# Kernel tuning notes

Hardware: AMD Instinct MI355X
Metric: run time of the kernel (lower is better)

Reference implementation:

```python
import jax, jax.numpy as jnp
import numpy as np

B, T, C, H = 4, 4096, 1024, 16

def setup_inputs() -> dict:
    key = jax.random.key(0)
    k1, k2, k3, k4 = jax.random.split(key, 4)
    return {
        "x": jax.random.normal(k1, (B, T, C), dtype=jnp.float32),
        "W_attn": jax.random.normal(k2, (C, C), dtype=jnp.float32) * 0.02,
        "b_attn": jnp.zeros((C,), dtype=jnp.float32),
        "W_proj": jax.random.normal(k3, (C, C), dtype=jnp.float32) * 0.02,
        "b_proj": jnp.zeros((C,), dtype=jnp.float32),
        "temp": jnp.ones((H, 1), dtype=jnp.float32),
        "n_head": H,
    }

def reference(x, W_attn, b_attn, W_proj, b_proj, temp, n_head):
    Bb, Tt, Cc = x.shape
    D = Cc // n_head
    # c_attn (torch Linear: x @ W.T + b)
    w = x @ W_attn.T + b_attn                         # (B,T,C)
    w = w.reshape(Bb, Tt, n_head, D).transpose(0, 2, 1, 3)  # (B,H,T,D)
    # F.normalize over token axis (dim=-2), eps=1e-12
    norm = jnp.maximum(jnp.sqrt(jnp.sum(w * w, axis=-2, keepdims=True)), 1e-12)
    w_normed = w / norm
    tmp = jnp.sum(w_normed ** 2, axis=-1) * temp      # (B,H,T) * (H,1) -> (B,H,T)
    Pi = jax.nn.softmax(tmp, axis=1)                  # softmax over heads
    Pi_prob = Pi / (jnp.sum(Pi, axis=-1, keepdims=True) + 1e-8)  # (B,H,T)
    dots = jnp.einsum('bht,bhtd->bhd', Pi_prob, w ** 2)          # (B,H,D)
    attn = 1.0 / (1.0 + dots)                         # (B,H,D)
    y = -(w * Pi[..., None]) * attn[:, :, None, :]    # (B,H,T,D)
    y = y.transpose(0, 2, 1, 3).reshape(Bb, Tt, Cc)
    return y @ W_proj.T + b_proj
```

## Files before the change

### kernel.cpp

```cpp
#include <hip/hip_runtime.h>
#include <hip/hip_bf16.h>

#define BB 4
#define TT 4096
#define CC 1024
#define HH 16
#define DD 64

typedef __attribute__((ext_vector_type(8))) short short8;
typedef __attribute__((ext_vector_type(8))) __bf16 bf16x8;
typedef __attribute__((ext_vector_type(4))) float f32x4;

static __device__ __forceinline__ unsigned short f2bf(float f) {
    unsigned int u = __builtin_bit_cast(unsigned int, f);
    unsigned int r = (u + 0x7FFFu + ((u >> 16) & 1u)) >> 16;
    return (unsigned short)r;
}
static __device__ __forceinline__ float bf2f(unsigned short h) {
    return __builtin_bit_cast(float, ((unsigned int)h) << 16);
}
static __device__ __forceinline__ bf16x8 cvt8(f32x4 a, f32x4 b) {
    bf16x8 r;
    r[0] = (__bf16)a[0]; r[1] = (__bf16)a[1]; r[2] = (__bf16)a[2]; r[3] = (__bf16)a[3];
    r[4] = (__bf16)b[0]; r[5] = (__bf16)b[1]; r[6] = (__bf16)b[2]; r[7] = (__bf16)b[3];
    return r;
}

__global__ void k_f32_to_bf16(const float* __restrict__ src,
                              unsigned short* __restrict__ dst, int n4) {
    int i = blockIdx.x * 256 + threadIdx.x;
    if (i >= n4) return;
    float4 v = ((const float4*)src)[i];
    ushort4 o;
    o.x = f2bf(v.x); o.y = f2bf(v.y); o.z = f2bf(v.z); o.w = f2bf(v.w);
    ((ushort4*)dst)[i] = o;
}

#define GBM 128
#define GBN 128
#define GBK 32

static __device__ __forceinline__ void stage_b16t(
    const unsigned short* __restrict__ Gbase, unsigned short* lbase,
    int k0, int K, int tid)
{
    #pragma unroll
    for (int q = 0; q < 2; ++q) {
        int c = q * 256 + tid;
        int r = c >> 2;
        int j = c & 3;
        int srcj = (j - (r >> 1)) & 3;
        const unsigned short* g = Gbase + (size_t)r * K + k0 + srcj * 8;
        __builtin_amdgcn_global_load_lds(
            (const __attribute__((address_space(1))) void*)g,
            (__attribute__((address_space(3))) void*)(lbase + c * 8), 16, 0, 0);
    }
}

static __device__ __forceinline__ void stage_a32t(
    const float* __restrict__ Gbase, unsigned short* lbase,
    int k0, int K, int tid)
{
    #pragma unroll
    for (int q = 0; q < 4; ++q) {
        int c = q * 256 + tid;
        int r = c >> 3;
        int j = c & 7;
        int srcj = (j - r) & 7;
        const float* g = Gbase + (size_t)r * K + k0 + srcj * 4;
        __builtin_amdgcn_global_load_lds(
            (const __attribute__((address_space(1))) void*)g,
            (__attribute__((address_space(3))) void*)(lbase + c * 8), 16, 0, 0);
    }
}

template<int MODE>
__global__ __launch_bounds__(256, 2)
void k_gemm128(const void* __restrict__ Asrc,
               const unsigned short* __restrict__ B,
               const float* __restrict__ bias,
               void* __restrict__ Cout,
               float* __restrict__ S,
               int M, int N, int K)
{
    constexpr int AREG = (MODE == 0) ? 8192 : 4096;
    __shared__ unsigned short lds[AREG + 4096];
    const int tid  = threadIdx.x;
    const int wave = tid >> 6;
    const int lane = tid & 63;
    const int wr = wave >> 1;
    const int wc = wave & 1;
    const int fr = lane & 15;
    const int hi = lane >> 4;

    const int wg  = blockIdx.x;
    const int swz = (wg & 7) * 128 + (wg >> 3);
    const int bn  = swz & 7;
    const int bm  = swz >> 3;
    const int b   = bm >> 5;

    const float* Af32 = (const float*)Asrc + (size_t)(bm * GBM) * K;
    const unsigned short* Ab16 = (const unsigned short*)Asrc + (size_t)(bm * GBM) * K;
    const unsigned short* Bbase = B +
        ((size_t)((MODE == 1 ? b * N : 0) + bn * GBN)) * K;

    const int nt = K / GBK;

    const int slB  = (hi + (fr >> 1)) & 3;
    const int aoff = (wr * 64 + fr) * 32 + slB * 8;
    const int boff = AREG + (wc * 64 + fr) * 32 + slB * 8;
    const int sl0  = (2 * hi + fr) & 7;
    const int sl1  = (2 * hi + 1 + fr) & 7;
    const int arowf = (wr * 64 + fr) * 32;

    f32x4 acc[4][4] = {};

    for (int kt = 0; kt < nt; ++kt) {
        const int k0 = kt * GBK;
        if (MODE == 0) stage_a32t(Af32, lds, k0, K, tid);
        else           stage_b16t(Ab16, lds, k0, K, tid);
        stage_b16t(Bbase, lds + AREG, k0, K, tid);
        __syncthreads();

        bf16x8 af[4]; short8 bfr[4];
        #pragma unroll
        for (int i = 0; i < 4; ++i) bfr[i] = *(const short8*)&lds[boff + i * 512];
        if (MODE == 0) {
            const float* fbuf = (const float*)lds;
            #pragma unroll
            for (int mi = 0; mi < 4; ++mi)
                af[mi] = cvt8(*(const f32x4*)&fbuf[arowf + mi * 512 + sl0 * 4],
                              *(const f32x4*)&fbuf[arowf + mi * 512 + sl1 * 4]);
        } else {
            #pragma unroll
            for (int mi = 0; mi < 4; ++mi)
                af[mi] = __builtin_bit_cast(bf16x8, *(const short8*)&lds[aoff + mi * 512]);
        }

        #pragma unroll
        for (int mi = 0; mi < 4; ++mi)
            #pragma unroll
            for (int ni = 0; ni < 4; ++ni)
                acc[mi][ni] = __builtin_amdgcn_mfma_f32_16x16x32_bf16(
                    af[mi], __builtin_bit_cast(bf16x8, bfr[ni]),
                    acc[mi][ni], 0, 0, 0);
        __syncthreads();
    }

    const int cg = fr;
    const int rg = hi * 4;
    float* sblk = (float*)&lds[0];
    if (MODE == 0) {
        if (tid < GBN) sblk[tid] = 0.f;
        __syncthreads();
    }
    float csum[4] = {};
    #pragma unroll
    for (int mi = 0; mi < 4; ++mi) {
        #pragma unroll
        for (int ni = 0; ni < 4; ++ni) {
            int col = bn * GBN + wc * 64 + ni * 16 + cg;
            float bv = bias[col];
            #pragma unroll
            for (int j = 0; j < 4; ++j) {
                int row = bm * GBM + wr * 64 + mi * 16 + rg + j;
                float v = acc[mi][ni][j] + bv;
                if (MODE == 0) {
                    ((unsigned short*)Cout)[(size_t)row * N + col] = f2bf(v);
                    csum[ni] += v * v;
                } else {
                    ((float*)Cout)[(size_t)row * N + col] = v;
                }
            }
        }
    }
    if (MODE == 0) {
        #pragma unroll
        for (int ni = 0; ni < 4; ++ni)
            atomicAdd(&sblk[wc * 64 + ni * 16 + cg], csum[ni]);
        __syncthreads();
        if (tid < GBN) atomicAdd(&S[b * CC + bn * GBN + tid], sblk[tid]);
    }
}

__global__ __launch_bounds__(256)
void k_row_softmax(unsigned short* __restrict__ w16, const float* __restrict__ S,
                   const float* __restrict__ temp,
                   float* __restrict__ dotsU, float* __restrict__ sumPi)
{
    __shared__ float dots_local[CC];
    __shared__ float sPi_local[HH];
    const int tid  = threadIdx.x;
    const int wave = tid >> 6;
    const int lane = tid & 63;
    const int bb   = blockIdx.x >> 7;
    const int tile = blockIdx.x & 127;

    for (int c = tid; c < CC; c += 256) dots_local[c] = 0.f;
    if (tid < HH) sPi_local[tid] = 0.f;
    __syncthreads();

    const int g3 = lane >> 3;
    const int li = lane & 7;

    float inv[2][8], tsc[2];
    #pragma unroll
    for (int q = 0; q < 2; ++q) {
        int c = q * 512 + lane * 8;
        const float4* sp = (const float4*)&S[bb * CC + c];
        float4 s0 = sp[0], s1 = sp[1];
        inv[q][0] = 1.f / fmaxf(s0.x, 1e-24f); inv[q][1] = 1.f / fmaxf(s0.y, 1e-24f);
        inv[q][2] = 1.f / fmaxf(s0.z, 1e-24f); inv[q][3] = 1.f / fmaxf(s0.w, 1e-24f);
        inv[q][4] = 1.f / fmaxf(s1.x, 1e-24f); inv[q][5] = 1.f / fmaxf(s1.y, 1e-24f);
        inv[q][6] = 1.f / fmaxf(s1.z, 1e-24f); inv[q][7] = 1.f / fmaxf(s1.w, 1e-24f);
        tsc[q] = temp[q * 8 + g3];
    }

    float dacc[2][8] = {};
    float sPiAcc[2] = {};

    for (int i = 0; i < 8; ++i) {
        int t = tile * 32 + wave * 8 + i;
        unsigned short* row = w16 + ((size_t)bb * TT + t) * CC;
        float wf[2][8];
        float pq[2];
        #pragma unroll
        for (int q = 0; q < 2; ++q) {
            short8 v = *(const short8*)&row[q * 512 + lane * 8];
            float s = 0.f;
            #pragma unroll
            for (int j = 0; j < 8; ++j) {
                wf[q][j] = bf2f((unsigned short)v[j]);
                s += wf[q][j] * wf[q][j] * inv[q][j];
            }
            pq[q] = s;
        }
        #pragma unroll
        for (int off = 1; off < 8; off <<= 1) {
            pq[0] += __shfl_xor(pq[0], off);
            pq[1] += __shfl_xor(pq[1], off);
        }
        pq[0] *= tsc[0]; pq[1] *= tsc[1];
        float mx = fmaxf(pq[0], pq[1]);
        mx = fmaxf(mx, __shfl_xor(mx, 8));
        mx = fmaxf(mx, __shfl_xor(mx, 16));
        mx = fmaxf(mx, __shfl_xor(mx, 32));
        float e0 = __expf(pq[0] - mx), e1 = __expf(pq[1] - mx);
        float ss = e0 + e1;
        ss += __shfl_xor(ss, 8);
        ss += __shfl_xor(ss, 16);
        ss += __shfl_xor(ss, 32);
        float rs = 1.f / ss;
        float piv[2] = { e0 * rs, e1 * rs };
        #pragma unroll
        for (int q = 0; q < 2; ++q) {
            short8 yo;
            #pragma unroll
            for (int j = 0; j < 8; ++j) {
                dacc[q][j] += piv[q] * wf[q][j] * wf[q][j];
                yo[j] = (short)f2bf(-wf[q][j] * piv[q]);
            }
            *(short8*)&row[q * 512 + lane * 8] = yo;
            if (li == 0) sPiAcc[q] += piv[q];
        }
    }

    #pragma unroll
    for (int q = 0; q < 2; ++q) {
        int c = q * 512 + lane * 8;
        #pragma unroll
        for (int j = 0; j < 8; ++j)
            atomicAdd(&dots_local[c + j], dacc[q][j]);
        if (li == 0) atomicAdd(&sPi_local[q * 8 + g3], sPiAcc[q]);
    }
    __syncthreads();
    for (int c = tid; c < CC; c += 256) atomicAdd(&dotsU[bb * CC + c], dots_local[c]);
    if (tid < HH) atomicAdd(&sumPi[bb * HH + tid], sPi_local[tid]);
}

__global__ void k_scale_wproj(const float* __restrict__ Wp,
                              const float* __restrict__ dotsU,
                              const float* __restrict__ sumPi,
                              unsigned short* __restrict__ out)
{
    int i = blockIdx.x * 256 + threadIdx.x;
    int bq  = i >> 18;
    int rem = i & 262143;
    int n   = rem >> 8;
    int cg  = (rem & 255) * 4;
    float4 wv = *(const float4*)&Wp[n * CC + cg];
    float4 du = *(const float4*)&dotsU[bq * CC + cg];
    float sp = sumPi[bq * HH + (cg >> 6)] + 1e-8f;
    float a0 = 1.f / (1.f + du.x / sp);
    float a1 = 1.f / (1.f + du.y / sp);
    float a2 = 1.f / (1.f + du.z / sp);
    float a3 = 1.f / (1.f + du.w / sp);
    ushort4 o;
    o.x = f2bf(wv.x * a0); o.y = f2bf(wv.y * a1);
    o.z = f2bf(wv.z * a2); o.w = f2bf(wv.w * a3);
    *(ushort4*)&out[((size_t)bq * CC + n) * CC + cg] = o;
}

extern "C" void kernel_launch(void* const* d_in, const int* in_sizes, int n_in,
                              void* d_out, int out_size, void* d_ws, size_t ws_size,
                              hipStream_t stream) {
    const float* x      = (const float*)d_in[0];
    const float* W_attn = (const float*)d_in[1];
    const float* b_attn = (const float*)d_in[2];
    const float* W_proj = (const float*)d_in[3];
    const float* b_proj = (const float*)d_in[4];
    const float* temp   = (const float*)d_in[5];

    char* ws = (char*)d_ws;
    unsigned short* w16   = (unsigned short*)(ws);
    unsigned short* Wa16  = (unsigned short*)(ws + 33554432);
    unsigned short* Wp16b = (unsigned short*)(ws + 35651584);
    float* S     = (float*)(ws + 44040192);
    float* dotsU = (float*)(ws + 44056576);
    float* sumPi = (float*)(ws + 44072960);

    k_f32_to_bf16<<<dim3(1024), dim3(256), 0, stream>>>(W_attn, Wa16, 262144);

    hipMemsetAsync(S, 0, 16384 + 16384 + 256, stream);

    k_gemm128<0><<<dim3(1024), dim3(256), 0, stream>>>(
        x, Wa16, b_attn, w16, S, BB * TT, CC, CC);

    k_row_softmax<<<dim3(512), dim3(256), 0, stream>>>(w16, S, temp, dotsU, sumPi);

    k_scale_wproj<<<dim3(4096), dim3(256), 0, stream>>>(W_proj, dotsU, sumPi, Wp16b);

    k_gemm128<1><<<dim3(1024), dim3(256), 0, stream>>>(
        w16, Wp16b, b_proj, d_out, nullptr, BB * TT, CC, CC);
}
```

Measured before the change: 152.4 us.

## Rewrite first GEMM with 256x256 tiles and triple-buffered async LDS pipeline

The first GEMM (x @ W_attn with fused column sum-of-squares) becomes a 512-thread kernel with 256x256 output tiles and a three-stage LDS ring. Global-to-LDS loads are issued two k-steps ahead and gated by vmcnt waits instead of full syncthreads. MFMA sections are wrapped in raised wave priority. The intent is to hide global load latency and raise arithmetic intensity per block, at the cost of a 144KB LDS footprint (one block per CU) and fewer blocks (256) to spread across CUs.

```diff
diff --git a/kernel.cpp b/kernel.cpp
--- a/kernel.cpp
+++ b/kernel.cpp
@@ -36,11 +36,144 @@
     ((ushort4*)dst)[i] = o;
 }
 
-#define GBM 128
-#define GBN 128
-#define GBK 32
-
-static __device__ __forceinline__ void stage_b16t(
+static __device__ __forceinline__ void stage_b16_512(
+    const unsigned short* __restrict__ Gbase, unsigned short* lbase,
+    int k0, int K, int wave, int lane)
+{
+    #pragma unroll
+    for (int q = 0; q < 2; ++q) {
+        int c = (wave * 2 + q) * 64 + lane;
+        int r = c >> 2;
+        int j = c & 3;
+        int srcj = (j - (r >> 1)) & 3;
+        const unsigned short* g = Gbase + (size_t)r * K + k0 + srcj * 8;
+        __builtin_amdgcn_global_load_lds(
+            (const __attribute__((address_space(1))) void*)g,
+            (__attribute__((address_space(3))) void*)(lbase + (wave * 2 + q) * 512),
+            16, 0, 0);
+    }
+}
+
+static __device__ __forceinline__ void stage_a32_512(
+    const float* __restrict__ Gbase, unsigned short* lbase,
+    int k0, int K, int wave, int lane)
+{
+    #pragma unroll
+    for (int q = 0; q < 4; ++q) {
+        int c = q * 512 + wave * 64 + lane;
+        int r = c >> 3;
+        int j = c & 7;
+        int srcj = (j - r) & 7;
+        const float* g = Gbase + (size_t)r * K + k0 + srcj * 4;
+        __builtin_amdgcn_global_load_lds(
+            (const __attribute__((address_space(1))) void*)g,
+            (__attribute__((address_space(3))) void*)(lbase + (q * 512 + wave * 64) * 8),
+            16, 0, 0);
+    }
+}
+
+__global__ __launch_bounds__(512, 2)
+void k_gemm1(const float* __restrict__ X,
+             const unsigned short* __restrict__ B,
+             const float* __restrict__ bias,
+             unsigned short* __restrict__ Cout,
+             float* __restrict__ S,
+             int M, int N, int K)
+{
+    __shared__ unsigned short lds[3][24576];
+    const int tid  = threadIdx.x;
+    const int wave = tid >> 6;
+    const int lane = tid & 63;
+    const int wr = wave >> 2, wc = wave & 3;
+    const int fr = lane & 15, hi = lane >> 4;
+
+    const int wg  = blockIdx.x;
+    const int swz = (wg & 7) * 32 + (wg >> 3);
+    const int bn  = swz & 3;
+    const int bm  = swz >> 2;
+    const int b   = bm >> 4;
+
+    const float* Af32 = X + (size_t)(bm * 256) * K;
+    const unsigned short* Bbase = B + (size_t)(bn * 256) * K;
+    const int nt = K / 32;
+
+    const int slB  = (hi + (fr >> 1)) & 3;
+    const int boff = 16384 + (wc * 64 + fr) * 32 + slB * 8;
+    const int sl0   = (2 * hi + fr) & 7;
+    const int sl1   = (2 * hi + 1 + fr) & 7;
+    const int arowf = (wr * 128 + fr) * 32;
+
+    f32x4 acc[8][4] = {};
+
+    stage_a32_512(Af32, lds[0],          0,  K, wave, lane);
+    stage_b16_512(Bbase, lds[0] + 16384, 0,  K, wave, lane);
+    stage_a32_512(Af32, lds[1],          32, K, wave, lane);
+    stage_b16_512(Bbase, lds[1] + 16384, 32, K, wave, lane);
+
+    int rb = 0;
+    for (int kt = 0; kt < nt; ++kt) {
+        const unsigned short* buf = lds[rb];
+        unsigned short* sbuf = lds[(rb == 0) ? 2 : rb - 1];
+        int ks = kt + 2; if (ks >= nt) ks = nt - 1;
+        asm volatile("s_waitcnt vmcnt(6)" ::: "memory");
+        __builtin_amdgcn_s_barrier();
+
+        bf16x8 af[8]; short8 bfr[4];
+        #pragma unroll
+        for (int i = 0; i < 4; ++i) bfr[i] = *(const short8*)&buf[boff + i * 512];
+        const float* fbuf = (const float*)buf;
+        #pragma unroll
+        for (int mi = 0; mi < 8; ++mi)
+            af[mi] = cvt8(*(const f32x4*)&fbuf[arowf + mi * 512 + sl0 * 4],
+                          *(const f32x4*)&fbuf[arowf + mi * 512 + sl1 * 4]);
+
+        stage_a32_512(Af32, sbuf,          ks * 32, K, wave, lane);
+        stage_b16_512(Bbase, sbuf + 16384, ks * 32, K, wave, lane);
+
+        __builtin_amdgcn_s_setprio(1);
+        #pragma unroll
+        for (int mi = 0; mi < 8; ++mi)
+            #pragma unroll
+            for (int ni = 0; ni < 4; ++ni)
+                acc[mi][ni] = __builtin_amdgcn_mfma_f32_16x16x32_bf16(
+                    af[mi], __builtin_bit_cast(bf16x8, bfr[ni]),
+                    acc[mi][ni], 0, 0, 0);
+        __builtin_amdgcn_s_setprio(0);
+
+        rb = (rb == 2) ? 0 : rb + 1;
+    }
+
+    __syncthreads();
+
+    const int cg = fr;
+    const int rg = hi * 4;
+    float* sblk = (float*)&lds[0][0];
+    if (tid < 256) sblk[tid] = 0.f;
+    __syncthreads();
+    float csum[4] = {};
+    #pragma unroll
+    for (int mi = 0; mi < 8; ++mi) {
+        #pragma unroll
+        for (int ni = 0; ni < 4; ++ni) {
+            int col = bn * 256 + wc * 64 + ni * 16 + cg;
+            float bv = bias[col];
+            #pragma unroll
+            for (int j = 0; j < 4; ++j) {
+                int row = bm * 256 + wr * 128 + mi * 16 + rg + j;
+                float v = acc[mi][ni][j] + bv;
+                Cout[(size_t)row * N + col] = f2bf(v);
+                csum[ni] += v * v;
+            }
+        }
+    }
+    #pragma unroll
+    for (int ni = 0; ni < 4; ++ni)
+        atomicAdd(&sblk[wc * 64 + ni * 16 + cg], csum[ni]);
+    __syncthreads();
+    if (tid < 256) atomicAdd(&S[b * CC + bn * 256 + tid], sblk[tid]);
+}
+
+static __device__ __forceinline__ void stage_b16_256(
     const unsigned short* __restrict__ Gbase, unsigned short* lbase,
     int k0, int K, int tid)
 {
@@ -57,41 +190,19 @@
     }
 }
 
-static __device__ __forceinline__ void stage_a32t(
-    const float* __restrict__ Gbase, unsigned short* lbase,
-    int k0, int K, int tid)
-{
-    #pragma unroll
-    for (int q = 0; q < 4; ++q) {
-        int c = q * 256 + tid;
-        int r = c >> 3;
-        int j = c & 7;
-        int srcj = (j - r) & 7;
-        const float* g = Gbase + (size_t)r * K + k0 + srcj * 4;
-        __builtin_amdgcn_global_load_lds(
-            (const __attribute__((address_space(1))) void*)g,
-            (__attribute__((address_space(3))) void*)(lbase + c * 8), 16, 0, 0);
-    }
-}
-
-template<int MODE>
 __global__ __launch_bounds__(256, 2)
-void k_gemm128(const void* __restrict__ Asrc,
-               const unsigned short* __restrict__ B,
-               const float* __restrict__ bias,
-               void* __restrict__ Cout,
-               float* __restrict__ S,
-               int M, int N, int K)
-{
-    constexpr int AREG = (MODE == 0) ? 8192 : 4096;
-    __shared__ unsigned short lds[AREG + 4096];
+void k_gemm2(const unsigned short* __restrict__ A,
+             const unsigned short* __restrict__ B,
+             const float* __restrict__ bias,
+             float* __restrict__ Cout,
+             int M, int N, int K)
+{
+    __shared__ unsigned short lds[8192];
     const int tid  = threadIdx.x;
     const int wave = tid >> 6;
     const int lane = tid & 63;
-    const int wr = wave >> 1;
-    const int wc = wave & 1;
-    const int fr = lane & 15;
-    const int hi = lane >> 4;
+    const int wr = wave >> 1, wc = wave & 1;
+    const int fr = lane & 15, hi = lane >> 4;
 
     const int wg  = blockIdx.x;
     const int swz = (wg & 7) * 128 + (wg >> 3);
@@ -99,43 +210,28 @@
     const int bm  = swz >> 3;
     const int b   = bm >> 5;
 
-    const float* Af32 = (const float*)Asrc + (size_t)(bm * GBM) * K;
-    const unsigned short* Ab16 = (const unsigned short*)Asrc + (size_t)(bm * GBM) * K;
-    const unsigned short* Bbase = B +
-        ((size_t)((MODE == 1 ? b * N : 0) + bn * GBN)) * K;
-
-    const int nt = K / GBK;
+    const unsigned short* Abase = A + (size_t)(bm * 128) * K;
+    const unsigned short* Bbase = B + ((size_t)(b * N + bn * 128)) * K;
+    const int nt = K / 32;
 
     const int slB  = (hi + (fr >> 1)) & 3;
     const int aoff = (wr * 64 + fr) * 32 + slB * 8;
-    const int boff = AREG + (wc * 64 + fr) * 32 + slB * 8;
-    const int sl0  = (2 * hi + fr) & 7;
-    const int sl1  = (2 * hi + 1 + fr) & 7;
-    const int arowf = (wr * 64 + fr) * 32;
+    const int boff = 4096 + (wc * 64 + fr) * 32 + slB * 8;
 
     f32x4 acc[4][4] = {};
 
     for (int kt = 0; kt < nt; ++kt) {
-        const int k0 = kt * GBK;
-        if (MODE == 0) stage_a32t(Af32, lds, k0, K, tid);
-        else           stage_b16t(Ab16, lds, k0, K, tid);
-        stage_b16t(Bbase, lds + AREG, k0, K, tid);
+        const int k0 = kt * 32;
+        stage_b16_256(Abase, lds,        k0, K, tid);
+        stage_b16_256(Bbase, lds + 4096, k0, K, tid);
         __syncthreads();
 
         bf16x8 af[4]; short8 bfr[4];
         #pragma unroll
         for (int i = 0; i < 4; ++i) bfr[i] = *(const short8*)&lds[boff + i * 512];
-        if (MODE == 0) {
-            const float* fbuf = (const float*)lds;
-            #pragma unroll
-            for (int mi = 0; mi < 4; ++mi)
-                af[mi] = cvt8(*(const f32x4*)&fbuf[arowf + mi * 512 + sl0 * 4],
-                              *(const f32x4*)&fbuf[arowf + mi * 512 + sl1 * 4]);
-        } else {
-            #pragma unroll
-            for (int mi = 0; mi < 4; ++mi)
-                af[mi] = __builtin_bit_cast(bf16x8, *(const short8*)&lds[aoff + mi * 512]);
-        }
+        #pragma unroll
+        for (int mi = 0; mi < 4; ++mi)
+            af[mi] = __builtin_bit_cast(bf16x8, *(const short8*)&lds[aoff + mi * 512]);
 
         #pragma unroll
         for (int mi = 0; mi < 4; ++mi)
@@ -149,37 +245,18 @@
 
     const int cg = fr;
     const int rg = hi * 4;
-    float* sblk = (float*)&lds[0];
-    if (MODE == 0) {
-        if (tid < GBN) sblk[tid] = 0.f;
-        __syncthreads();
-    }
-    float csum[4] = {};
     #pragma unroll
     for (int mi = 0; mi < 4; ++mi) {
         #pragma unroll
         for (int ni = 0; ni < 4; ++ni) {
-            int col = bn * GBN + wc * 64 + ni * 16 + cg;
+            int col = bn * 128 + wc * 64 + ni * 16 + cg;
             float bv = bias[col];
             #pragma unroll
             for (int j = 0; j < 4; ++j) {
-                int row = bm * GBM + wr * 64 + mi * 16 + rg + j;
-                float v = acc[mi][ni][j] + bv;
-                if (MODE == 0) {
-                    ((unsigned short*)Cout)[(size_t)row * N + col] = f2bf(v);
-                    csum[ni] += v * v;
-                } else {
-                    ((float*)Cout)[(size_t)row * N + col] = v;
-                }
+                int row = bm * 128 + wr * 64 + mi * 16 + rg + j;
+                Cout[(size_t)row * N + col] = acc[mi][ni][j] + bv;
             }
         }
-    }
-    if (MODE == 0) {
-        #pragma unroll
-        for (int ni = 0; ni < 4; ++ni)
-            atomicAdd(&sblk[wc * 64 + ni * 16 + cg], csum[ni]);
-        __syncthreads();
-        if (tid < GBN) atomicAdd(&S[b * CC + bn * GBN + tid], sblk[tid]);
     }
 }
 
@@ -323,13 +400,13 @@
 
     hipMemsetAsync(S, 0, 16384 + 16384 + 256, stream);
 
-    k_gemm128<0><<<dim3(1024), dim3(256), 0, stream>>>(
+    k_gemm1<<<dim3(256), dim3(512), 0, stream>>>(
         x, Wa16, b_attn, w16, S, BB * TT, CC, CC);
 
     k_row_softmax<<<dim3(512), dim3(256), 0, stream>>>(w16, S, temp, dotsU, sumPi);
 
     k_scale_wproj<<<dim3(4096), dim3(256), 0, stream>>>(W_proj, dotsU, sumPi, Wp16b);
 
-    k_gemm128<1><<<dim3(1024), dim3(256), 0, stream>>>(
-        w16, Wp16b, b_proj, d_out, nullptr, BB * TT, CC, CC);
-}
+    k_gemm2<<<dim3(1024), dim3(256), 0, stream>>>(
+        w16, Wp16b, b_proj, (float*)d_out, BB * TT, CC, CC);
+}
```

Measured after the change: 128.8 us. -15.5%, faster.
